# Performance work log

Measured on AMD Instinct MI355X. Metric: run time of the kernel, lower is better.

## Reference

```python
import jax, jax.numpy as jnp
import numpy as np

QMAX = 127.0

def setup_inputs() -> dict:
    key = jax.random.key(0)
    k1, k2, k3 = jax.random.split(key, 3)
    x = jax.random.normal(k1, (4, 2048, 2048), dtype=jnp.float32)
    weight = jax.random.normal(k2, (2048, 2048), dtype=jnp.float32)  # [out, in]
    bias = jax.random.normal(k3, (2048,), dtype=jnp.float32)
    return {"x": x, "weight": weight, "bias": bias}

def _quantize(t):
    # per-tensor abs-max symmetric int8 quantization
    scale = jnp.max(jnp.abs(t)) / QMAX
    q = jnp.clip(jnp.round(t / scale), -128.0, 127.0).astype(jnp.int8)
    return q, scale

def reference(x, weight, bias):
    orig_shape = x.shape
    x2 = x.reshape(-1, x.shape[-1])                      # [tokens, in]
    x_q, in_scale = _quantize(x2)
    w_q, w_scale = _quantize(weight)                     # weight: [out, in]
    # int8 GEMM accumulated in int32: [tokens, out]
    acc = jnp.matmul(x_q.astype(jnp.int32), w_q.T.astype(jnp.int32))
    # dequant (output_scale = 1.0) + bias epilogue
    out = acc.astype(jnp.float32) * (in_scale * w_scale) + bias[None, :]
    return out.reshape(*orig_shape[:-1], weight.shape[0])
```

## Files before the change

kernel.cpp:

```cpp
#include <hip/hip_runtime.h>
#include <stdint.h>

#define GK 2048
#define GN 2048
#define GM 8192

#define NVX (GM * (unsigned)GK / 4)
#define NVW (GN * (unsigned)GK / 4)

#define XBLK 1024
#define WBLK 256
#define QXBLK 4096
#define QWBLK 1024
#define NT (GK / 128)

typedef int i32x4 __attribute__((ext_vector_type(4)));

__device__ __forceinline__ float amax4(float4 v) {
    return fmaxf(fmaxf(fabsf(v.x), fabsf(v.y)), fmaxf(fabsf(v.z), fabsf(v.w)));
}

__global__ __launch_bounds__(256) void absmax_kernel(
    const float4* __restrict__ xv, const float4* __restrict__ wv,
    float* __restrict__ partial)
{
    const bool isx = blockIdx.x < XBLK;
    const float4* __restrict__ src = isx ? xv : wv;
    const unsigned n      = isx ? NVX : NVW;
    const unsigned b0     = isx ? blockIdx.x : blockIdx.x - XBLK;
    const unsigned stride = (isx ? XBLK : WBLK) * 256u;

    unsigned i = b0 * 256u + threadIdx.x;
    float m = 0.f;
    for (; i + 3u * stride < n; i += 4u * stride) {
        float4 a = src[i];
        float4 b = src[i + stride];
        float4 c = src[i + 2u * stride];
        float4 d = src[i + 3u * stride];
        m = fmaxf(m, fmaxf(fmaxf(amax4(a), amax4(b)),
                           fmaxf(amax4(c), amax4(d))));
    }
    for (; i < n; i += stride) m = fmaxf(m, amax4(src[i]));

    #pragma unroll
    for (int off = 32; off > 0; off >>= 1)
        m = fmaxf(m, __shfl_xor(m, off, 64));

    __shared__ float sm[4];
    const int wid = threadIdx.x >> 6;
    if ((threadIdx.x & 63) == 0) sm[wid] = m;
    __syncthreads();
    if (threadIdx.x == 0)
        partial[blockIdx.x] = fmaxf(fmaxf(sm[0], sm[1]), fmaxf(sm[2], sm[3]));
}

__device__ __forceinline__ void reduce_scales(const float* __restrict__ partial,
                                              int tid, float* ax_out, float* aw_out)
{
    __shared__ float smx[4], smw[4];
    float mx = 0.f, mw = 0.f;
    if (tid < 256) {
        mx = fmaxf(fmaxf(partial[tid], partial[tid + 256]),
                   fmaxf(partial[tid + 512], partial[tid + 768]));
        mw = partial[1024 + tid];
        #pragma unroll
        for (int off = 32; off > 0; off >>= 1) {
            mx = fmaxf(mx, __shfl_xor(mx, off, 64));
            mw = fmaxf(mw, __shfl_xor(mw, off, 64));
        }
        if ((tid & 63) == 0) { smx[tid >> 6] = mx; smw[tid >> 6] = mw; }
    }
    __syncthreads();
    *ax_out = fmaxf(fmaxf(smx[0], smx[1]), fmaxf(smx[2], smx[3]));
    *aw_out = fmaxf(fmaxf(smw[0], smw[1]), fmaxf(smw[2], smw[3]));
}

__device__ __forceinline__ signed char quant1(float v, float s) {
    float r = rintf(v / s);
    r = fminf(fmaxf(r, -128.f), 127.f);
    return (signed char)(int)r;
}

__device__ __forceinline__ char4 quantv(float4 v, float s) {
    char4 q;
    q.x = quant1(v.x, s); q.y = quant1(v.y, s);
    q.z = quant1(v.z, s); q.w = quant1(v.w, s);
    return q;
}

__global__ __launch_bounds__(256) void quant_kernel(
    const float4* __restrict__ xv, const float4* __restrict__ wv,
    const float* __restrict__ partial,
    char4* __restrict__ xq, char4* __restrict__ wq)
{
    float ax, aw;
    reduce_scales(partial, threadIdx.x, &ax, &aw);

    const bool isx = blockIdx.x < QXBLK;
    const float s = (isx ? ax : aw) / 127.0f;
    const float4* __restrict__ src = isx ? xv : wv;
    char4* __restrict__ dst        = isx ? xq : wq;
    const unsigned b0     = isx ? blockIdx.x : blockIdx.x - QXBLK;
    const unsigned stride = (isx ? QXBLK : QWBLK) * 256u;
    const unsigned t      = b0 * 256u + threadIdx.x;

    float4 a = src[t];
    float4 b = src[t + stride];
    float4 c = src[t + 2u * stride];
    float4 d = src[t + 3u * stride];
    dst[t]               = quantv(a, s);
    dst[t + stride]      = quantv(b, s);
    dst[t + 2u * stride] = quantv(c, s);
    dst[t + 3u * stride] = quantv(d, s);
}

__global__ __launch_bounds__(512, 2) void gemm_kernel(
    const signed char* __restrict__ Aq,
    const signed char* __restrict__ Bq,
    const float* __restrict__ bias,
    const float* __restrict__ partial,
    float* __restrict__ out)
{
    __shared__ signed char lds[131072];

    const int tid  = threadIdx.x;
    const int lane = tid & 63;
    const int wid  = tid >> 6;
    const int wr   = wid >> 2;
    const int wc   = wid & 3;

    const int wgid = ((blockIdx.x & 7) << 5) | (blockIdx.x >> 3);
    const int bn   = wgid & 7;
    const int bm   = wgid >> 3;

    float ax, aw;
    reduce_scales(partial, tid, &ax, &aw);
    const float s = (ax / 127.0f) * (aw / 127.0f);

    const int srcslot = (tid & 7) ^ ((tid >> 3) & 7);
    const signed char* aSrc[4]; const signed char* bSrc[4];
    int aDst[4], bDst[4];
    #pragma unroll
    for (int he = 0; he < 4; ++he) {
        const int h = he >> 1, e = he & 1;
        const int r = h * 128 + e * 64 + (tid >> 3);
        aSrc[he] = Aq + (long)(bm * 256 + r) * GK + srcslot * 16;
        bSrc[he] = Bq + (long)(bn * 256 + r) * GK + srcslot * 16;
        aDst[he] = h * 16384 + e * 8192 + tid * 16;
        bDst[he] = 32768 + h * 16384 + e * 8192 + tid * 16;
    }

    const int lcol = lane & 15;
    const int g0   = lane >> 4;
    const int r7   = lcol & 7;
    int aOff[8], bOff[4];
    #pragma unroll
    for (int mf = 0; mf < 8; ++mf) aOff[mf] = (wr * 128 + mf * 16 + lcol) * 128;
    #pragma unroll
    for (int n = 0; n < 4; ++n)    bOff[n] = 32768 + (wc * 64 + n * 16 + lcol) * 128;

    i32x4 acc[8][4] = {};

    #pragma unroll
    for (int he = 0; he < 4; ++he) {
        __builtin_amdgcn_global_load_lds(
            (const __attribute__((address_space(1))) void*)aSrc[he],
            (__attribute__((address_space(3))) void*)(lds + aDst[he]), 16, 0, 0);
        __builtin_amdgcn_global_load_lds(
            (const __attribute__((address_space(1))) void*)bSrc[he],
            (__attribute__((address_space(3))) void*)(lds + bDst[he]), 16, 0, 0);
    }
    __syncthreads();

    for (int t = 0; t < NT; ++t) {
        const signed char* buf = lds + (t & 1) * 65536;
        signed char* nbuf      = lds + ((t & 1) ^ 1) * 65536;
        const long knext = (long)(t + 1) * 128;
        i32x4 bf[4];

        #pragma unroll
        for (int ph = 0; ph < 4; ++ph) {
            const int mq = ph & 1, ks = ph >> 1;
            const int sw = ((ks * 4 + g0) ^ r7) << 4;

            if ((ph & 1) == 0) {
                #pragma unroll
                for (int n = 0; n < 4; ++n)
                    bf[n] = *(const i32x4*)(buf + bOff[n] + sw);
            }
            i32x4 af[4];
            #pragma unroll
            for (int m = 0; m < 4; ++m)
                af[m] = *(const i32x4*)(buf + aOff[mq * 4 + m] + sw);

            if (ph == 0 && t + 1 < NT) {
                #pragma unroll
                for (int he = 0; he < 4; ++he)
                    __builtin_amdgcn_global_load_lds(
                        (const __attribute__((address_space(1))) void*)(aSrc[he] + knext),
                        (__attribute__((address_space(3))) void*)(nbuf + aDst[he]), 16, 0, 0);
            }
            if (ph == 1 && t + 1 < NT) {
                #pragma unroll
                for (int he = 0; he < 4; ++he)
                    __builtin_amdgcn_global_load_lds(
                        (const __attribute__((address_space(1))) void*)(bSrc[he] + knext),
                        (__attribute__((address_space(3))) void*)(nbuf + bDst[he]), 16, 0, 0);
            }

            __builtin_amdgcn_s_barrier();
            __builtin_amdgcn_s_setprio(1);
            #pragma unroll
            for (int m = 0; m < 4; ++m)
                #pragma unroll
                for (int n = 0; n < 4; ++n)
                    acc[mq * 4 + m][n] = __builtin_amdgcn_mfma_i32_16x16x64_i8(
                        af[m], bf[n], acc[mq * 4 + m][n], 0, 0, 0);
            __builtin_amdgcn_s_setprio(0);

            if (ph == 3 && t + 1 < NT) {
                asm volatile("s_waitcnt vmcnt(0)" ::: "memory");
                __builtin_amdgcn_sched_barrier(0);
            }
            __builtin_amdgcn_s_barrier();
        }
    }

    const int orow0 = bm * 256 + wr * 128 + (lane >> 4) * 4;
    const int ocol0 = bn * 256 + wc * 64 + lcol;
    #pragma unroll
    for (int n = 0; n < 4; ++n) {
        const int col = ocol0 + n * 16;
        const float bv = bias[col];
        #pragma unroll
        for (int mf = 0; mf < 8; ++mf) {
            const int row = orow0 + mf * 16;
            #pragma unroll
            for (int i = 0; i < 4; ++i)
                out[(long)(row + i) * GN + col] = (float)acc[mf][n][i] * s + bv;
        }
    }
}

extern "C" void kernel_launch(void* const* d_in, const int* in_sizes, int n_in,
                              void* d_out, int out_size, void* d_ws, size_t ws_size,
                              hipStream_t stream) {
    const float* x    = (const float*)d_in[0];
    const float* w    = (const float*)d_in[1];
    const float* bias = (const float*)d_in[2];
    float* out = (float*)d_out;

    const size_t need = 8192 + (size_t)GM * GK + (size_t)GN * GK;
    if (ws_size < need) return;

    float* partial   = (float*)d_ws + 4;
    signed char* xq  = (signed char*)d_ws + 8192;
    signed char* wq  = xq + (size_t)GM * GK;

    absmax_kernel<<<XBLK + WBLK, 256, 0, stream>>>(
        (const float4*)x, (const float4*)w, partial);
    quant_kernel<<<QXBLK + QWBLK, 256, 0, stream>>>(
        (const float4*)x, (const float4*)w, partial, (char4*)xq, (char4*)wq);
    gemm_kernel<<<(GM / 256) * (GN / 256), 512, 0, stream>>>(
        xq, wq, bias, partial, out);
}
```

Baseline: 175.0 us.

## Restructure GEMM main loop into quadrant phases with staggered half-tile prefetch

```diff
diff --git a/kernel.cpp b/kernel.cpp
--- a/kernel.cpp
+++ b/kernel.cpp
@@ -150,96 +150,151 @@
         bDst[he] = 32768 + h * 16384 + e * 8192 + tid * 16;
     }
 
+    #define STAGE_A(hh, buf, koff)                                             \
+        { __builtin_amdgcn_global_load_lds(                                    \
+              (const __attribute__((address_space(1))) void*)(aSrc[2*(hh)] + (koff)),   \
+              (__attribute__((address_space(3))) void*)((buf) + aDst[2*(hh)]), 16,0,0); \
+          __builtin_amdgcn_global_load_lds(                                    \
+              (const __attribute__((address_space(1))) void*)(aSrc[2*(hh)+1] + (koff)), \
+              (__attribute__((address_space(3))) void*)((buf) + aDst[2*(hh)+1]),16,0,0);}
+    #define STAGE_B(hh, buf, koff)                                             \
+        { __builtin_amdgcn_global_load_lds(                                    \
+              (const __attribute__((address_space(1))) void*)(bSrc[2*(hh)] + (koff)),   \
+              (__attribute__((address_space(3))) void*)((buf) + bDst[2*(hh)]), 16,0,0); \
+          __builtin_amdgcn_global_load_lds(                                    \
+              (const __attribute__((address_space(1))) void*)(bSrc[2*(hh)+1] + (koff)), \
+              (__attribute__((address_space(3))) void*)((buf) + bDst[2*(hh)+1]),16,0,0);}
+
     const int lcol = lane & 15;
     const int g0   = lane >> 4;
     const int r7   = lcol & 7;
     int aOff[8], bOff[4];
     #pragma unroll
-    for (int mf = 0; mf < 8; ++mf) aOff[mf] = (wr * 128 + mf * 16 + lcol) * 128;
-    #pragma unroll
-    for (int n = 0; n < 4; ++n)    bOff[n] = 32768 + (wc * 64 + n * 16 + lcol) * 128;
+    for (int m = 0; m < 8; ++m) {
+        const int row = (m < 4) ? (wr * 64 + m * 16 + lcol)
+                                : (128 + wr * 64 + (m - 4) * 16 + lcol);
+        aOff[m] = row * 128;
+    }
+    #pragma unroll
+    for (int n = 0; n < 4; ++n) {
+        const int row = (n < 2) ? (wc * 32 + n * 16 + lcol)
+                                : (128 + wc * 32 + (n - 2) * 16 + lcol);
+        bOff[n] = 32768 + row * 128;
+    }
 
     i32x4 acc[8][4] = {};
 
-    #pragma unroll
-    for (int he = 0; he < 4; ++he) {
-        __builtin_amdgcn_global_load_lds(
-            (const __attribute__((address_space(1))) void*)aSrc[he],
-            (__attribute__((address_space(3))) void*)(lds + aDst[he]), 16, 0, 0);
-        __builtin_amdgcn_global_load_lds(
-            (const __attribute__((address_space(1))) void*)bSrc[he],
-            (__attribute__((address_space(3))) void*)(lds + bDst[he]), 16, 0, 0);
-    }
+    STAGE_B(0, lds, 0) STAGE_B(1, lds, 0) STAGE_A(0, lds, 0) STAGE_A(1, lds, 0)
     __syncthreads();
 
     for (int t = 0; t < NT; ++t) {
         const signed char* buf = lds + (t & 1) * 65536;
         signed char* nbuf      = lds + ((t & 1) ^ 1) * 65536;
-        const long knext = (long)(t + 1) * 128;
-        i32x4 bf[4];
-
-        #pragma unroll
-        for (int ph = 0; ph < 4; ++ph) {
-            const int mq = ph & 1, ks = ph >> 1;
-            const int sw = ((ks * 4 + g0) ^ r7) << 4;
-
-            if ((ph & 1) == 0) {
+        const long kn = (long)(t + 1) * 128;
+        const bool more = (t + 1 < NT);
+        i32x4 a0[4][2], a1[4][2], b0[2][2], b1[2][2];
+
+        const int sw0 = (g0 ^ r7) << 4;
+        const int sw1 = ((4 + g0) ^ r7) << 4;
+
+        #pragma unroll
+        for (int m = 0; m < 4; ++m) {
+            a0[m][0] = *(const i32x4*)(buf + aOff[m] + sw0);
+            a0[m][1] = *(const i32x4*)(buf + aOff[m] + sw1);
+        }
+        #pragma unroll
+        for (int n = 0; n < 2; ++n) {
+            b0[n][0] = *(const i32x4*)(buf + bOff[n] + sw0);
+            b0[n][1] = *(const i32x4*)(buf + bOff[n] + sw1);
+        }
+        if (more) STAGE_B(0, nbuf, kn)
+        __builtin_amdgcn_s_barrier();
+        __builtin_amdgcn_s_setprio(1);
+        #pragma unroll
+        for (int m = 0; m < 4; ++m)
+            #pragma unroll
+            for (int n = 0; n < 2; ++n)
                 #pragma unroll
-                for (int n = 0; n < 4; ++n)
-                    bf[n] = *(const i32x4*)(buf + bOff[n] + sw);
-            }
-            i32x4 af[4];
-            #pragma unroll
-            for (int m = 0; m < 4; ++m)
-                af[m] = *(const i32x4*)(buf + aOff[mq * 4 + m] + sw);
-
-            if (ph == 0 && t + 1 < NT) {
+                for (int k = 0; k < 2; ++k)
+                    acc[m][n] = __builtin_amdgcn_mfma_i32_16x16x64_i8(
+                        a0[m][k], b0[n][k], acc[m][n], 0, 0, 0);
+        __builtin_amdgcn_s_setprio(0);
+        __builtin_amdgcn_s_barrier();
+
+        #pragma unroll
+        for (int n = 0; n < 2; ++n) {
+            b1[n][0] = *(const i32x4*)(buf + bOff[n + 2] + sw0);
+            b1[n][1] = *(const i32x4*)(buf + bOff[n + 2] + sw1);
+        }
+        if (more) STAGE_B(1, nbuf, kn)
+        asm volatile("s_waitcnt vmcnt(4)" ::: "memory");
+        __builtin_amdgcn_sched_barrier(0);
+        __builtin_amdgcn_s_barrier();
+        __builtin_amdgcn_s_setprio(1);
+        #pragma unroll
+        for (int m = 0; m < 4; ++m)
+            #pragma unroll
+            for (int n = 0; n < 2; ++n)
                 #pragma unroll
-                for (int he = 0; he < 4; ++he)
-                    __builtin_amdgcn_global_load_lds(
-                        (const __attribute__((address_space(1))) void*)(aSrc[he] + knext),
-                        (__attribute__((address_space(3))) void*)(nbuf + aDst[he]), 16, 0, 0);
-            }
-            if (ph == 1 && t + 1 < NT) {
+                for (int k = 0; k < 2; ++k)
+                    acc[m][n + 2] = __builtin_amdgcn_mfma_i32_16x16x64_i8(
+                        a0[m][k], b1[n][k], acc[m][n + 2], 0, 0, 0);
+        __builtin_amdgcn_s_setprio(0);
+        __builtin_amdgcn_s_barrier();
+
+        #pragma unroll
+        for (int m = 0; m < 4; ++m) {
+            a1[m][0] = *(const i32x4*)(buf + aOff[m + 4] + sw0);
+            a1[m][1] = *(const i32x4*)(buf + aOff[m + 4] + sw1);
+        }
+        if (more) STAGE_A(0, nbuf, kn)
+        __builtin_amdgcn_s_barrier();
+        __builtin_amdgcn_s_setprio(1);
+        #pragma unroll
+        for (int m = 0; m < 4; ++m)
+            #pragma unroll
+            for (int n = 0; n < 2; ++n)
                 #pragma unroll
-                for (int he = 0; he < 4; ++he)
-                    __builtin_amdgcn_global_load_lds(
-                        (const __attribute__((address_space(1))) void*)(bSrc[he] + knext),
-                        (__attribute__((address_space(3))) void*)(nbuf + bDst[he]), 16, 0, 0);
-            }
-
-            __builtin_amdgcn_s_barrier();
-            __builtin_amdgcn_s_setprio(1);
-            #pragma unroll
-            for (int m = 0; m < 4; ++m)
+                for (int k = 0; k < 2; ++k)
+                    acc[m + 4][n] = __builtin_amdgcn_mfma_i32_16x16x64_i8(
+                        a1[m][k], b0[n][k], acc[m + 4][n], 0, 0, 0);
+        __builtin_amdgcn_s_setprio(0);
+        __builtin_amdgcn_s_barrier();
+
+        if (more) STAGE_A(1, nbuf, kn)
+        asm volatile("s_waitcnt vmcnt(2)" ::: "memory");
+        __builtin_amdgcn_sched_barrier(0);
+        __builtin_amdgcn_s_barrier();
+        __builtin_amdgcn_s_setprio(1);
+        #pragma unroll
+        for (int m = 0; m < 4; ++m)
+            #pragma unroll
+            for (int n = 0; n < 2; ++n)
                 #pragma unroll
-                for (int n = 0; n < 4; ++n)
-                    acc[mq * 4 + m][n] = __builtin_amdgcn_mfma_i32_16x16x64_i8(
-                        af[m], bf[n], acc[mq * 4 + m][n], 0, 0, 0);
-            __builtin_amdgcn_s_setprio(0);
-
-            if (ph == 3 && t + 1 < NT) {
-                asm volatile("s_waitcnt vmcnt(0)" ::: "memory");
-                __builtin_amdgcn_sched_barrier(0);
-            }
-            __builtin_amdgcn_s_barrier();
-        }
-    }
-
-    const int orow0 = bm * 256 + wr * 128 + (lane >> 4) * 4;
-    const int ocol0 = bn * 256 + wc * 64 + lcol;
+                for (int k = 0; k < 2; ++k)
+                    acc[m + 4][n + 2] = __builtin_amdgcn_mfma_i32_16x16x64_i8(
+                        a1[m][k], b1[n][k], acc[m + 4][n + 2], 0, 0, 0);
+        __builtin_amdgcn_s_setprio(0);
+        __builtin_amdgcn_s_barrier();
+    }
+
     #pragma unroll
     for (int n = 0; n < 4; ++n) {
-        const int col = ocol0 + n * 16;
+        const int col = bn * 256 + ((n < 2) ? (wc * 32 + n * 16)
+                                            : (128 + wc * 32 + (n - 2) * 16)) + lcol;
         const float bv = bias[col];
         #pragma unroll
-        for (int mf = 0; mf < 8; ++mf) {
-            const int row = orow0 + mf * 16;
+        for (int m = 0; m < 8; ++m) {
+            const int row0 = bm * 256 + ((m < 4) ? (wr * 64 + m * 16)
+                                                 : (128 + wr * 64 + (m - 4) * 16))
+                             + (lane >> 4) * 4;
             #pragma unroll
             for (int i = 0; i < 4; ++i)
-                out[(long)(row + i) * GN + col] = (float)acc[mf][n][i] * s + bv;
-        }
-    }
+                out[(long)(row0 + i) * GN + col] = (float)acc[m][n][i] * s + bv;
+        }
+    }
+    #undef STAGE_A
+    #undef STAGE_B
 }
 
 extern "C" void kernel_launch(void* const* d_in, const int* in_sizes, int n_in,
```

After: 176.3 us. No clear change (+0.8%).

## Simplify GEMM main loop: issue all prefetches upfront, drop per-phase barriers

Applied to the files above, without the earlier changes.

```diff
diff --git a/kernel.cpp b/kernel.cpp
--- a/kernel.cpp
+++ b/kernel.cpp
@@ -150,80 +150,58 @@
         bDst[he] = 32768 + h * 16384 + e * 8192 + tid * 16;
     }
 
+    #define STAGE_ALL(buf, koff)                                               \
+        { _Pragma("unroll")                                                    \
+          for (int he = 0; he < 4; ++he) {                                     \
+            __builtin_amdgcn_global_load_lds(                                  \
+              (const __attribute__((address_space(1))) void*)(aSrc[he] + (koff)),       \
+              (__attribute__((address_space(3))) void*)((buf) + aDst[he]), 16, 0, 0);   \
+            __builtin_amdgcn_global_load_lds(                                  \
+              (const __attribute__((address_space(1))) void*)(bSrc[he] + (koff)),       \
+              (__attribute__((address_space(3))) void*)((buf) + bDst[he]), 16, 0, 0);   \
+          } }
+
     const int lcol = lane & 15;
     const int g0   = lane >> 4;
     const int r7   = lcol & 7;
     int aOff[8], bOff[4];
     #pragma unroll
-    for (int mf = 0; mf < 8; ++mf) aOff[mf] = (wr * 128 + mf * 16 + lcol) * 128;
-    #pragma unroll
-    for (int n = 0; n < 4; ++n)    bOff[n] = 32768 + (wc * 64 + n * 16 + lcol) * 128;
+    for (int m = 0; m < 8; ++m) aOff[m] = (wr * 128 + m * 16 + lcol) * 128;
+    #pragma unroll
+    for (int n = 0; n < 4; ++n) bOff[n] = 32768 + (wc * 64 + n * 16 + lcol) * 128;
 
     i32x4 acc[8][4] = {};
 
-    #pragma unroll
-    for (int he = 0; he < 4; ++he) {
-        __builtin_amdgcn_global_load_lds(
-            (const __attribute__((address_space(1))) void*)aSrc[he],
-            (__attribute__((address_space(3))) void*)(lds + aDst[he]), 16, 0, 0);
-        __builtin_amdgcn_global_load_lds(
-            (const __attribute__((address_space(1))) void*)bSrc[he],
-            (__attribute__((address_space(3))) void*)(lds + bDst[he]), 16, 0, 0);
-    }
+    STAGE_ALL(lds, 0)
     __syncthreads();
 
     for (int t = 0; t < NT; ++t) {
         const signed char* buf = lds + (t & 1) * 65536;
         signed char* nbuf      = lds + ((t & 1) ^ 1) * 65536;
-        const long knext = (long)(t + 1) * 128;
-        i32x4 bf[4];
+
+        if (t + 1 < NT) STAGE_ALL(nbuf, (long)(t + 1) * 128)
+        __builtin_amdgcn_sched_barrier(0);
 
         #pragma unroll
-        for (int ph = 0; ph < 4; ++ph) {
-            const int mq = ph & 1, ks = ph >> 1;
+        for (int ks = 0; ks < 2; ++ks) {
             const int sw = ((ks * 4 + g0) ^ r7) << 4;
-
-            if ((ph & 1) == 0) {
+            i32x4 bf[4];
+            #pragma unroll
+            for (int n = 0; n < 4; ++n)
+                bf[n] = *(const i32x4*)(buf + bOff[n] + sw);
+            #pragma unroll
+            for (int m = 0; m < 8; ++m) {
+                const i32x4 af = *(const i32x4*)(buf + aOff[m] + sw);
                 #pragma unroll
                 for (int n = 0; n < 4; ++n)
-                    bf[n] = *(const i32x4*)(buf + bOff[n] + sw);
+                    acc[m][n] = __builtin_amdgcn_mfma_i32_16x16x64_i8(
+                        af, bf[n], acc[m][n], 0, 0, 0);
             }
-            i32x4 af[4];
-            #pragma unroll
-            for (int m = 0; m < 4; ++m)
-                af[m] = *(const i32x4*)(buf + aOff[mq * 4 + m] + sw);
-
-            if (ph == 0 && t + 1 < NT) {
-                #pragma unroll
-                for (int he = 0; he < 4; ++he)
-                    __builtin_amdgcn_global_load_lds(
-                        (const __attribute__((address_space(1))) void*)(aSrc[he] + knext),
-                        (__attribute__((address_space(3))) void*)(nbuf + aDst[he]), 16, 0, 0);
-            }
-            if (ph == 1 && t + 1 < NT) {
-                #pragma unroll
-                for (int he = 0; he < 4; ++he)
-                    __builtin_amdgcn_global_load_lds(
-                        (const __attribute__((address_space(1))) void*)(bSrc[he] + knext),
-                        (__attribute__((address_space(3))) void*)(nbuf + bDst[he]), 16, 0, 0);
-            }
-
-            __builtin_amdgcn_s_barrier();
-            __builtin_amdgcn_s_setprio(1);
-            #pragma unroll
-            for (int m = 0; m < 4; ++m)
-                #pragma unroll
-                for (int n = 0; n < 4; ++n)
-                    acc[mq * 4 + m][n] = __builtin_amdgcn_mfma_i32_16x16x64_i8(
-                        af[m], bf[n], acc[mq * 4 + m][n], 0, 0, 0);
-            __builtin_amdgcn_s_setprio(0);
-
-            if (ph == 3 && t + 1 < NT) {
-                asm volatile("s_waitcnt vmcnt(0)" ::: "memory");
-                __builtin_amdgcn_sched_barrier(0);
-            }
-            __builtin_amdgcn_s_barrier();
         }
+
+        asm volatile("s_waitcnt vmcnt(0)" ::: "memory");
+        __builtin_amdgcn_sched_barrier(0);
+        __builtin_amdgcn_s_barrier();
     }
 
     const int orow0 = bm * 256 + wr * 128 + (lane >> 4) * 4;
@@ -233,13 +211,14 @@
         const int col = ocol0 + n * 16;
         const float bv = bias[col];
         #pragma unroll
-        for (int mf = 0; mf < 8; ++mf) {
-            const int row = orow0 + mf * 16;
+        for (int m = 0; m < 8; ++m) {
+            const int row = orow0 + m * 16;
             #pragma unroll
             for (int i = 0; i < 4; ++i)
-                out[(long)(row + i) * GN + col] = (float)acc[mf][n][i] * s + bv;
+                out[(long)(row + i) * GN + col] = (float)acc[m][n][i] * s + bv;
         }
     }
+    #undef STAGE_ALL
 }
 
 extern "C" void kernel_launch(void* const* d_in, const int* in_sizes, int n_in,
```

After: 178.5 us. +2.0%, slower.
